# Kernel optimization log

Hardware: AMD Instinct MI355X
Metric: run time of the kernel (lower is better)

Reference implementation:

```python
import jax, jax.numpy as jnp
import numpy as np

B, T, D, H, E, K = 8, 4096, 768, 3072, 4, 2


def setup_inputs() -> dict:
    key = jax.random.key(0)
    ks = jax.random.split(key, 7)
    s = 0.02
    return {
        "x": jax.random.normal(ks[0], (B, T, D), dtype=jnp.float32),
        "router_w": jax.random.normal(ks[1], (D, E), dtype=jnp.float32) * s,
        "router_b": jnp.zeros((E,), dtype=jnp.float32),
        "W1": jax.random.normal(ks[2], (E, D, H), dtype=jnp.float32) * s,
        "b1": jnp.zeros((E, H), dtype=jnp.float32),
        "W2": jax.random.normal(ks[3], (E, H, D), dtype=jnp.float32) * s,
        "b2": jnp.zeros((E, D), dtype=jnp.float32),
    }


def reference(x, router_w, router_b, W1, b1, W2, b2):
    # Router: softmax over experts, then top-k selection.
    logits = jnp.einsum('btd,de->bte', x, router_w) + router_b        # [B,T,E]
    probs = jax.nn.softmax(logits, axis=-1)                           # [B,T,E]
    topk_probs, topk_idx = jax.lax.top_k(probs, K)                    # [B,T,K]

    # Per-expert combine weight: sum of top-k probs assigned to expert e.
    onehot = jax.nn.one_hot(topk_idx, E, dtype=x.dtype)               # [B,T,K,E]
    w = jnp.einsum('btk,btke->bte', topk_probs, onehot)               # [B,T,E]

    # Expert FFNs (exact-erf GELU matches torch F.gelu default).
    out = jnp.zeros_like(x)
    for e in range(E):
        h = jax.nn.gelu(jnp.einsum('btd,dh->bth', x, W1[e]) + b1[e], approximate=False)
        y = jnp.einsum('bth,hd->btd', h, W2[e]) + b2[e]
        out = out + w[..., e:e + 1] * y

    # Load-balance loss: expert assignment counts (non-differentiable, from int idx).
    counts = onehot.sum(axis=(0, 1, 2))                               # [E]
    token_fraction = counts / counts.sum()
    router_prob_mean = probs.mean(axis=(0, 1))                        # [E]
    load_balance_loss = E * jnp.sum(router_prob_mean * token_fraction)
    return out, load_balance_loss
```

## Files before the change

### kernel.cpp

```cpp
#include <hip/hip_runtime.h>
#include <hip/hip_bf16.h>
#include <hip/hip_fp16.h>

#define N_TOK 32768
#define D_DIM 768
#define H_DIM 3072
#define E_NUM 4
#define MT_PAD (N_TOK + 512)

#define TILE_E 4096

typedef _Float16 f16_t;
typedef _Float16 f16x8 __attribute__((ext_vector_type(8)));
typedef float f32x4 __attribute__((ext_vector_type(4)));

__device__ __forceinline__ f16_t f2h(float f) { return (f16_t)f; }

__device__ __forceinline__ void gload16(const void* g, void* l) {
  __builtin_amdgcn_global_load_lds(
      (const __attribute__((address_space(1))) void*)g,
      (__attribute__((address_space(3))) void*)l,
      16, 0, 0);
}

__device__ __forceinline__ void pipe_barrier() {
  asm volatile("" ::: "memory");
  __builtin_amdgcn_sched_barrier(0);
  __builtin_amdgcn_s_barrier();
  __builtin_amdgcn_sched_barrier(0);
  asm volatile("" ::: "memory");
}

__device__ __forceinline__ int xcd_swizzle(int f, int nwg) {
  const int q = nwg >> 3, r = nwg & 7;
  const int xcd = f & 7, pos = f >> 3;
  return (xcd < r ? xcd * (q + 1) : r * (q + 1) + (xcd - r) * q) + pos;
}


__global__ __launch_bounds__(256) void fill_kernel(unsigned* __restrict__ idx0,
                                                   unsigned* __restrict__ idx1) {
  const int t = blockIdx.x * 256 + threadIdx.x;
  for (int i = t; i < MT_PAD; i += gridDim.x * 256) {
    idx0[i] = 0xFFFFFFFFu;
    idx1[i] = 0xFFFFFFFFu;
  }
}

__global__ __launch_bounds__(256) void transform_kernel(
    const float* __restrict__ in, f16_t* __restrict__ outT,
    int R, int C, int NT, int KT) {
  __shared__ float tile[32][33];
  const int ez = blockIdx.z;
  in += (size_t)ez * R * C;
  const int c0 = blockIdx.x * 32, r0 = blockIdx.y * 32;
  const int tc = threadIdx.x & 31, tr = threadIdx.x >> 5;
#pragma unroll
  for (int i = 0; i < 32; i += 8)
    tile[tr + i][tc] = in[(size_t)(r0 + tr + i) * C + c0 + tc];
  __syncthreads();
  const int kt = r0 >> 5, g = tc >> 3, kk = tc & 7;
#pragma unroll
  for (int i = 0; i < 32; i += 8) {
    const int n = c0 + tr + i;
    const int nt = n >> 7, rl = n & 127;
    outT[(((size_t)(ez * NT + nt)) * KT + kt) * TILE_E + g * 1024 + rl * 8 + kk]
        = f2h(tile[tc][tr + i]);
  }
}

__global__ __launch_bounds__(256) void router_kernel(
    const float* __restrict__ x, const float* __restrict__ rw, const float* __restrict__ rb,
    float* __restrict__ wcomb, int* __restrict__ pairinfo,
    float* __restrict__ psum_part, int* __restrict__ cnt_part,
    int* __restrict__ cnt0_part, int* __restrict__ cnt1_part) {
  __shared__ float rwT[E_NUM][D_DIM];
  __shared__ float prW[4][E_NUM];
  __shared__ int   cnW[4][E_NUM];
  __shared__ int   cn0W[4][E_NUM];
  __shared__ int   cn1W[4][E_NUM];
  const int tid = threadIdx.x;
  for (int i = tid; i < D_DIM * E_NUM; i += 256) {
    int k = i >> 2, e = i & 3;
    rwT[e][k] = rw[i];
  }
  __syncthreads();
  const int lane = tid & 63, wv_ = tid >> 6;
  float pacc[E_NUM] = {0.f, 0.f, 0.f, 0.f};
  int   cacc[E_NUM] = {0, 0, 0, 0};
  int   c0acc[E_NUM] = {0, 0, 0, 0};
  int   c1acc[E_NUM] = {0, 0, 0, 0};
  const int tok0 = blockIdx.x * 32 + wv_ * 8;
  for (int t = 0; t < 8; ++t) {
    const int m = tok0 + t;
    const float* xr = x + (size_t)m * D_DIM;
    float s0 = 0.f, s1 = 0.f, s2 = 0.f, s3 = 0.f;
#pragma unroll
    for (int i = 0; i < D_DIM / 64; ++i) {
      int k = lane + i * 64;
      float xv = xr[k];
      s0 += xv * rwT[0][k]; s1 += xv * rwT[1][k];
      s2 += xv * rwT[2][k]; s3 += xv * rwT[3][k];
    }
#pragma unroll
    for (int off = 32; off >= 1; off >>= 1) {
      s0 += __shfl_xor(s0, off); s1 += __shfl_xor(s1, off);
      s2 += __shfl_xor(s2, off); s3 += __shfl_xor(s3, off);
    }
    if (lane == 0) {
      float lg[4] = {s0 + rb[0], s1 + rb[1], s2 + rb[2], s3 + rb[3]};
      float mx = fmaxf(fmaxf(lg[0], lg[1]), fmaxf(lg[2], lg[3]));
      float p[4]; float den = 0.f;
#pragma unroll
      for (int e = 0; e < 4; ++e) { p[e] = expf(lg[e] - mx); den += p[e]; }
      float inv = 1.f / den;
#pragma unroll
      for (int e = 0; e < 4; ++e) p[e] *= inv;
      int i1 = 0;
#pragma unroll
      for (int e = 1; e < 4; ++e) if (p[e] > p[i1]) i1 = e;
      int i2 = (i1 == 0) ? 1 : 0;
#pragma unroll
      for (int e = 0; e < 4; ++e) if (e != i1 && p[e] > p[i2]) i2 = e;
      float4 wvout;
      wvout.x = (0 == i1 || 0 == i2) ? p[0] : 0.f;
      wvout.y = (1 == i1 || 1 == i2) ? p[1] : 0.f;
      wvout.z = (2 == i1 || 2 == i2) ? p[2] : 0.f;
      wvout.w = (3 == i1 || 3 == i2) ? p[3] : 0.f;
      ((float4*)wcomb)[m] = wvout;
      const int emin = (i1 < i2) ? i1 : i2;
      const int emax = (i1 < i2) ? i2 : i1;
      pairinfo[m] = emin | (emax << 4);
      c0acc[emin]++; c1acc[emax]++;
#pragma unroll
      for (int e = 0; e < 4; ++e) pacc[e] += p[e];
      cacc[i1]++; cacc[i2]++;
    }
  }
  if (lane == 0) {
#pragma unroll
    for (int e = 0; e < 4; ++e) {
      prW[wv_][e] = pacc[e]; cnW[wv_][e] = cacc[e];
      cn0W[wv_][e] = c0acc[e]; cn1W[wv_][e] = c1acc[e];
    }
  }
  __syncthreads();
  if (tid < 4) {
    float ps = prW[0][tid] + prW[1][tid] + prW[2][tid] + prW[3][tid];
    int   cs = cnW[0][tid] + cnW[1][tid] + cnW[2][tid] + cnW[3][tid];
    psum_part[blockIdx.x * 4 + tid] = ps;
    cnt_part[blockIdx.x * 4 + tid]  = cs;
    cnt0_part[blockIdx.x * 4 + tid] = cn0W[0][tid] + cn0W[1][tid] + cn0W[2][tid] + cn0W[3][tid];
    cnt1_part[blockIdx.x * 4 + tid] = cn1W[0][tid] + cn1W[1][tid] + cn1W[2][tid] + cn1W[3][tid];
  }
}

__global__ void loss_kernel(const float* __restrict__ psum_part,
                            const int* __restrict__ cnt_part,
                            float* __restrict__ loss_out, int nblk) {
  const int lane = threadIdx.x;
  float ps[4] = {0.f, 0.f, 0.f, 0.f};
  int   cs[4] = {0, 0, 0, 0};
  for (int r = lane; r < nblk; r += 64) {
#pragma unroll
    for (int e = 0; e < 4; ++e) { ps[e] += psum_part[r * 4 + e]; cs[e] += cnt_part[r * 4 + e]; }
  }
#pragma unroll
  for (int off = 32; off >= 1; off >>= 1) {
#pragma unroll
    for (int e = 0; e < 4; ++e) {
      ps[e] += __shfl_xor(ps[e], off);
      cs[e] += __shfl_xor(cs[e], off);
    }
  }
  if (lane == 0) {
    float loss = 0.f;
#pragma unroll
    for (int e = 0; e < 4; ++e) {
      float mean = ps[e] / (float)N_TOK;
      float frac = (float)cs[e] / (float)(N_TOK * 2);
      loss += mean * frac;
    }
    loss_out[0] = 4.f * loss;
  }
}

__global__ __launch_bounds__(256) void setup_kernel(const int* __restrict__ cnt0_part,
                                                    const int* __restrict__ cnt1_part,
                                                    int* __restrict__ meta, int nblk) {
  __shared__ int sh[8][32];
  const int ch = threadIdx.x >> 5, ln = threadIdx.x & 31;
  const int* src = (ch < 4) ? cnt0_part : cnt1_part;
  const int e = ch & 3;
  int s = 0;
  for (int b = ln; b < nblk; b += 32) s += src[b * 4 + e];
  sh[ch][ln] = s;
  __syncthreads();
  if (threadIdx.x == 0) {
    int c[8];
    for (int c2 = 0; c2 < 8; ++c2) {
      int t = 0;
      for (int l = 0; l < 32; ++l) t += sh[c2][l];
      c[c2] = t;
    }
    int pb = 0; meta[8] = 0;
    for (int e2 = 0; e2 < 4; ++e2) { pb += (c[e2] + 127) & ~127; meta[9 + e2] = pb; }
    pb = 0; meta[13] = 0;
    for (int e2 = 0; e2 < 4; ++e2) { pb += (c[4 + e2] + 127) & ~127; meta[14 + e2] = pb; }
    for (int e2 = 0; e2 < 4; ++e2) { meta[18 + e2] = meta[8 + e2]; meta[22 + e2] = meta[13 + e2]; }
  }
}

__global__ __launch_bounds__(256) void scatter_kernel(const int* __restrict__ pairinfo,
                                                      int* __restrict__ meta,
                                                      unsigned* __restrict__ idx0,
                                                      unsigned* __restrict__ idx1) {
  __shared__ int wcnt[2][4][4];
  __shared__ int blkbase[2][4];
  const int tid = threadIdx.x, lane = tid & 63, wv = tid >> 6;
  const int t = blockIdx.x * 256 + tid;
  const int info = pairinfo[t];
  const int esel0 = info & 15, esel1 = info >> 4;
  int rank0 = 0, rank1 = 0;
#pragma unroll
  for (int e = 0; e < 4; ++e) {
    unsigned long long m0 = __ballot(esel0 == e);
    if (esel0 == e) rank0 = __popcll(m0 & ((1ull << lane) - 1ull));
    unsigned long long m1 = __ballot(esel1 == e);
    if (esel1 == e) rank1 = __popcll(m1 & ((1ull << lane) - 1ull));
    if (lane == 0) { wcnt[0][wv][e] = __popcll(m0); wcnt[1][wv][e] = __popcll(m1); }
  }
  __syncthreads();
  int wbase0 = 0, wbase1 = 0;
  for (int w = 0; w < wv; ++w) { wbase0 += wcnt[0][w][esel0]; wbase1 += wcnt[1][w][esel1]; }
  if (tid < 8) {
    const int p = tid >> 2, e = tid & 3;
    const int tot = wcnt[p][0][e] + wcnt[p][1][e] + wcnt[p][2][e] + wcnt[p][3][e];
    blkbase[p][e] = atomicAdd(&meta[(p ? 22 : 18) + e], tot);
  }
  __syncthreads();
  idx0[blkbase[0][esel0] + wbase0 + rank0] = (unsigned)t;
  idx1[blkbase[1][esel1] + wbase1 + rank1] = (unsigned)t;
}

__global__ __launch_bounds__(256) void gather_kernel(
    const float* __restrict__ x, const unsigned* __restrict__ idx_p,
    f16_t* __restrict__ xg, int srow) {
  __shared__ unsigned idx_s[128];
  const int tid = threadIdx.x, mt = blockIdx.x;
  if (tid < 128) {
    const int gr = srow + mt * 128 + tid;
    idx_s[tid] = (gr < MT_PAD) ? idx_p[gr] : 0xFFFFFFFFu;
  }
  __syncthreads();
  f16_t* dst = xg + (size_t)mt * 24 * TILE_E;
  for (int i = tid; i < 128 * 96; i += 256) {
    const int r = i / 96, grp = i - r * 96;
    const unsigned v = idx_s[r];
    const float* src = x + (size_t)((v < N_TOK) ? v : 0u) * D_DIM + grp * 8;
    float4 f0 = ((const float4*)src)[0];
    float4 f1 = ((const float4*)src)[1];
    f16x8 h;
    h[0] = f2h(f0.x); h[1] = f2h(f0.y); h[2] = f2h(f0.z); h[3] = f2h(f0.w);
    h[4] = f2h(f1.x); h[5] = f2h(f1.y); h[6] = f2h(f1.z); h[7] = f2h(f1.w);
    const int kt = grp >> 2, g = grp & 3;
    *(f16x8*)&dst[(size_t)kt * TILE_E + g * 1024 + r * 8] = h;
  }
}

#define BM 128
#define BN 128
#define BK 32

__global__ __launch_bounds__(256, 4) void gemm1_kernel(
    const f16_t* __restrict__ xg, const f16_t* __restrict__ W1T,
    const float* __restrict__ b1, const int* __restrict__ pb_p,
    f16_t* __restrict__ HwP, int srow) {
  __shared__ __align__(16) f16_t As[2][TILE_E];
  __shared__ __align__(16) f16_t Bs[2][TILE_E];
  const int tid = threadIdx.x, lane = tid & 63, wid = tid >> 6;
  const int wg = xcd_swizzle(blockIdx.x, gridDim.x);
  const int ntile = wg % 24, mtile = wg / 24;
  const int m128 = srow + mtile * BM;
  if (m128 >= pb_p[4]) return;
  int e = 0;
  while (e < 3 && m128 >= pb_p[e + 1]) ++e;
  const int n0 = ntile * BN;

  const f16_t* abase = xg + (size_t)mtile * 24 * TILE_E + lane * 8;
  const f16_t* bbase = W1T + (size_t)(e * 24 + ntile) * 24 * TILE_E + lane * 8;

  auto stage = [&](int buf, int kt) {
    const f16_t* a = abase + (size_t)kt * TILE_E;
    const f16_t* b = bbase + (size_t)kt * TILE_E;
    gload16(a + wid * 512,        &As[buf][wid * 512]);
    gload16(a + 2048 + wid * 512, &As[buf][2048 + wid * 512]);
    gload16(b + wid * 512,        &Bs[buf][wid * 512]);
    gload16(b + 2048 + wid * 512, &Bs[buf][2048 + wid * 512]);
  };

  const int wr = wid >> 1, wc = wid & 1;
  f32x4 acc[4][4] = {};

  float b1v[4];
#pragma unroll
  for (int nf = 0; nf < 4; ++nf)
    b1v[nf] = b1[e * H_DIM + n0 + wc * 64 + nf * 16 + (lane & 15)];

  stage(0, 0);
  stage(1, 1);
  int cur = 0;
  const int NT = D_DIM / BK;
  for (int t = 0; t < NT; ++t) {
    if (t + 1 < NT) { asm volatile("s_waitcnt vmcnt(4)" ::: "memory"); }
    else            { asm volatile("s_waitcnt vmcnt(0)" ::: "memory"); }
    pipe_barrier();
    const f16x8* Av = (const f16x8*)As[cur];
    const f16x8* Bv = (const f16x8*)Bs[cur];
    const int gsel = (lane >> 4) * 128;
    f16x8 a[4], b[4];
#pragma unroll
    for (int mf = 0; mf < 4; ++mf) a[mf] = Av[gsel + wr * 64 + mf * 16 + (lane & 15)];
#pragma unroll
    for (int nf = 0; nf < 4; ++nf) b[nf] = Bv[gsel + wc * 64 + nf * 16 + (lane & 15)];
#pragma unroll
    for (int mf = 0; mf < 4; ++mf)
#pragma unroll
      for (int nf = 0; nf < 4; ++nf)
        acc[mf][nf] = __builtin_amdgcn_mfma_f32_16x16x32_f16(a[mf], b[nf], acc[mf][nf], 0, 0, 0);
    pipe_barrier();
    if (t + 2 < NT) stage(cur, t + 2);
    cur ^= 1;
  }

  const int colb = wc * 64 + (lane & 15);
#pragma unroll
  for (int mf = 0; mf < 4; ++mf) {
    const int rowb = wr * 64 + mf * 16 + ((lane >> 4) << 2);
#pragma unroll
    for (int nf = 0; nf < 4; ++nf) {
      const int col = n0 + colb + nf * 16;
      const int kt = col >> 5, g = (col >> 3) & 3, kk = col & 7;
#pragma unroll
      for (int j = 0; j < 4; ++j) {
        const int row = rowb + j;
        float v = acc[mf][nf][j] + b1v[nf];
        float gel = 0.5f * v * (1.0f + erff(v * 0.70710678118654752440f));
        HwP[((size_t)(mtile * 96 + kt)) * TILE_E + g * 1024 + row * 8 + kk] = f2h(gel);
      }
    }
  }
}

__global__ __launch_bounds__(256, 4) void gemm2_kernel(
    const f16_t* __restrict__ HwP, const f16_t* __restrict__ W2T,
    const float* __restrict__ b2, const float* __restrict__ wcomb,
    const unsigned* __restrict__ idx_p, const int* __restrict__ pb_p,
    float* __restrict__ out, int srow, int doAdd) {
  __shared__ __align__(16) f16_t As[2][TILE_E];
  __shared__ __align__(16) f16_t Bs[2][TILE_E];
  __shared__ unsigned idx_s[BM];
  __shared__ float w_s[BM];
  const int tid = threadIdx.x, lane = tid & 63, wid = tid >> 6;
  const int wg = xcd_swizzle(blockIdx.x, gridDim.x);
  const int ntile = wg % 6, mtile = wg / 6;
  const int m128 = srow + mtile * BM;
  if (m128 >= pb_p[4]) return;
  int e = 0;
  while (e < 3 && m128 >= pb_p[e + 1]) ++e;
  const int n0 = ntile * BN;

  if (tid < BM) idx_s[tid] = idx_p[m128 + tid];
  __syncthreads();
  if (tid < BM) {
    unsigned v = idx_s[tid];
    w_s[tid] = (v < N_TOK) ? wcomb[v * 4 + e] : 0.f;
  }

  const f16_t* abase = HwP + (size_t)mtile * 96 * TILE_E + lane * 8;
  const f16_t* bbase = W2T + (size_t)(e * 6 + ntile) * 96 * TILE_E + lane * 8;

  auto stage = [&](int buf, int kt) {
    const f16_t* a = abase + (size_t)kt * TILE_E;
    const f16_t* b = bbase + (size_t)kt * TILE_E;
    gload16(a + wid * 512,        &As[buf][wid * 512]);
    gload16(a + 2048 + wid * 512, &As[buf][2048 + wid * 512]);
    gload16(b + wid * 512,        &Bs[buf][wid * 512]);
    gload16(b + 2048 + wid * 512, &Bs[buf][2048 + wid * 512]);
  };

  const int wr = wid >> 1, wc = wid & 1;
  f32x4 acc[4][4] = {};

  float b2v[4];
#pragma unroll
  for (int nf = 0; nf < 4; ++nf)
    b2v[nf] = b2[e * D_DIM + n0 + wc * 64 + nf * 16 + (lane & 15)];

  stage(0, 0);
  stage(1, 1);
  int cur = 0;
  const int NT = H_DIM / BK;
  for (int t = 0; t < NT; ++t) {
    if (t + 1 < NT) { asm volatile("s_waitcnt vmcnt(4)" ::: "memory"); }
    else            { asm volatile("s_waitcnt vmcnt(0)" ::: "memory"); }
    pipe_barrier();
    const f16x8* Av = (const f16x8*)As[cur];
    const f16x8* Bv = (const f16x8*)Bs[cur];
    const int gsel = (lane >> 4) * 128;
    f16x8 a[4], b[4];
#pragma unroll
    for (int mf = 0; mf < 4; ++mf) a[mf] = Av[gsel + wr * 64 + mf * 16 + (lane & 15)];
#pragma unroll
    for (int nf = 0; nf < 4; ++nf) b[nf] = Bv[gsel + wc * 64 + nf * 16 + (lane & 15)];
#pragma unroll
    for (int mf = 0; mf < 4; ++mf)
#pragma unroll
      for (int nf = 0; nf < 4; ++nf)
        acc[mf][nf] = __builtin_amdgcn_mfma_f32_16x16x32_f16(a[mf], b[nf], acc[mf][nf], 0, 0, 0);
    pipe_barrier();
    if (t + 2 < NT) stage(cur, t + 2);
    cur ^= 1;
  }

  const int colb = wc * 64 + (lane & 15);
#pragma unroll
  for (int mf = 0; mf < 4; ++mf) {
    const int rowb = wr * 64 + mf * 16 + ((lane >> 4) << 2);
#pragma unroll
    for (int nf = 0; nf < 4; ++nf) {
      const int col = n0 + colb + nf * 16;
#pragma unroll
      for (int j = 0; j < 4; ++j) {
        const int row = rowb + j;
        const unsigned v = idx_s[row];
        if (v < N_TOK) {
          float contrib = w_s[row] * (acc[mf][nf][j] + b2v[nf]);
          float* po = out + (size_t)v * D_DIM + col;
          if (doAdd) *po += contrib; else *po = contrib;
        }
      }
    }
  }
}

extern "C" void kernel_launch(void* const* d_in, const int* in_sizes, int n_in,
                              void* d_out, int out_size, void* d_ws, size_t ws_size,
                              hipStream_t stream) {
  const float* x  = (const float*)d_in[0];
  const float* rw = (const float*)d_in[1];
  const float* rb = (const float*)d_in[2];
  const float* W1 = (const float*)d_in[3];
  const float* b1 = (const float*)d_in[4];
  const float* W2 = (const float*)d_in[5];
  const float* b2 = (const float*)d_in[6];
  float* out = (float*)d_out;

  char* ws = (char*)d_ws;
  size_t off = 0;
  auto alloc = [&](size_t bytes) -> void* {
    void* p = ws + off;
    off = (off + bytes + 255) & ~(size_t)255;
    return p;
  };
  f16_t* W1T = (f16_t*)alloc((size_t)E_NUM * D_DIM * H_DIM * sizeof(f16_t));
  f16_t* W2T = (f16_t*)alloc((size_t)E_NUM * D_DIM * H_DIM * sizeof(f16_t));
  float* wcomb = (float*)alloc((size_t)N_TOK * E_NUM * sizeof(float));
  float* psum_part = (float*)alloc((size_t)(N_TOK / 32) * 4 * sizeof(float));
  int*   cnt_part  = (int*)alloc((size_t)(N_TOK / 32) * 4 * sizeof(int));
  int*   cnt0_part = (int*)alloc((size_t)(N_TOK / 32) * 4 * sizeof(int));
  int*   cnt1_part = (int*)alloc((size_t)(N_TOK / 32) * 4 * sizeof(int));
  int*   pairinfo  = (int*)alloc((size_t)N_TOK * sizeof(int));
  int*   meta      = (int*)alloc(32 * sizeof(int));
  unsigned* idx0   = (unsigned*)alloc((size_t)MT_PAD * sizeof(unsigned));
  unsigned* idx1   = (unsigned*)alloc((size_t)MT_PAD * sizeof(unsigned));

  size_t avail = (ws_size > off) ? ws_size - off : 0;
  int hwrows = (int)(avail / 7680);
  if (hwrows > MT_PAD) hwrows = MT_PAD;
  hwrows &= ~127;
  if (hwrows < 128) hwrows = 128;
  const int chunks = (MT_PAD + hwrows - 1) / hwrows;
  f16_t* xg  = (f16_t*)(ws + off);
  f16_t* HwP = (f16_t*)(ws + off + (size_t)hwrows * D_DIM * sizeof(f16_t));

  const int nblk = N_TOK / 32;

  fill_kernel<<<128, 256, 0, stream>>>(idx0, idx1);
  transform_kernel<<<dim3(H_DIM / 32, D_DIM / 32, E_NUM), 256, 0, stream>>>(W1, W1T, D_DIM, H_DIM, 24, 24);
  transform_kernel<<<dim3(D_DIM / 32, H_DIM / 32, E_NUM), 256, 0, stream>>>(W2, W2T, H_DIM, D_DIM, 6, 96);
  router_kernel<<<nblk, 256, 0, stream>>>(x, rw, rb, wcomb, pairinfo,
                                          psum_part, cnt_part, cnt0_part, cnt1_part);
  loss_kernel<<<1, 64, 0, stream>>>(psum_part, cnt_part, out + (size_t)N_TOK * D_DIM, nblk);
  setup_kernel<<<1, 256, 0, stream>>>(cnt0_part, cnt1_part, meta, nblk);
  scatter_kernel<<<N_TOK / 256, 256, 0, stream>>>(pairinfo, meta, idx0, idx1);

  for (int pass = 0; pass < 2; ++pass) {
    const unsigned* ip = pass ? idx1 : idx0;
    const int* pbp = meta + (pass ? 13 : 8);
    for (int c = 0; c < chunks; ++c) {
      const int srow = c * hwrows;
      gather_kernel<<<hwrows / BM, 256, 0, stream>>>(x, ip, xg, srow);
      gemm1_kernel<<<(hwrows / BM) * 24, 256, 0, stream>>>(xg, W1T, b1, pbp, HwP, srow);
      gemm2_kernel<<<(hwrows / BM) * 6, 256, 0, stream>>>(HwP, W2T, b2, wcomb, ip, pbp, out, srow, pass);
    }
  }
}
```

Measured before the change: 1.094 ms.

## Use 256-row M tiles for second-pass down-projection GEMM with 512-thread blocks

Adds a gemm2b kernel used on the second routing pass. It processes 256 token rows per block with 8 waves, so each staged W2 tile is reused across twice as many rows. Expert segment padding and chunk sizes are raised to multiples of 256 so no tile straddles two experts. The extra padding adds some wasted rows, and the larger blocks use more LDS, which may lower occupancy.

```diff
diff --git a/kernel.cpp b/kernel.cpp
--- a/kernel.cpp
+++ b/kernel.cpp
@@ -6,7 +6,7 @@
 #define D_DIM 768
 #define H_DIM 3072
 #define E_NUM 4
-#define MT_PAD (N_TOK + 512)
+#define MT_PAD (N_TOK + 1024)
 
 #define TILE_E 4096
 
@@ -204,9 +204,9 @@
       c[c2] = t;
     }
     int pb = 0; meta[8] = 0;
-    for (int e2 = 0; e2 < 4; ++e2) { pb += (c[e2] + 127) & ~127; meta[9 + e2] = pb; }
+    for (int e2 = 0; e2 < 4; ++e2) { pb += (c[e2] + 255) & ~255; meta[9 + e2] = pb; }
     pb = 0; meta[13] = 0;
-    for (int e2 = 0; e2 < 4; ++e2) { pb += (c[4 + e2] + 127) & ~127; meta[14 + e2] = pb; }
+    for (int e2 = 0; e2 < 4; ++e2) { pb += (c[4 + e2] + 255) & ~255; meta[14 + e2] = pb; }
     for (int e2 = 0; e2 < 4; ++e2) { meta[18 + e2] = meta[8 + e2]; meta[22 + e2] = meta[13 + e2]; }
   }
 }
@@ -438,6 +438,98 @@
           float contrib = w_s[row] * (acc[mf][nf][j] + b2v[nf]);
           float* po = out + (size_t)v * D_DIM + col;
           if (doAdd) *po += contrib; else *po = contrib;
+        }
+      }
+    }
+  }
+}
+
+__global__ __launch_bounds__(512, 4) void gemm2b_kernel(
+    const f16_t* __restrict__ HwP, const f16_t* __restrict__ W2T,
+    const float* __restrict__ b2, const float* __restrict__ wcomb,
+    const unsigned* __restrict__ idx_p, const int* __restrict__ pb_p,
+    float* __restrict__ out, int srow) {
+  __shared__ __align__(16) f16_t As[2][2 * TILE_E];
+  __shared__ __align__(16) f16_t Bs[2][TILE_E];
+  __shared__ unsigned idx_s[256];
+  __shared__ float w_s[256];
+  const int tid = threadIdx.x, lane = tid & 63, wid = tid >> 6;
+  const int wg = xcd_swizzle(blockIdx.x, gridDim.x);
+  const int ntile = wg % 6, mtile = wg / 6;
+  const int m256 = srow + mtile * 256;
+  if (m256 >= pb_p[4]) return;
+  int e = 0;
+  while (e < 3 && m256 >= pb_p[e + 1]) ++e;
+  const int n0 = ntile * BN;
+
+  if (tid < 256) idx_s[tid] = idx_p[m256 + tid];
+  __syncthreads();
+  if (tid < 256) {
+    unsigned v = idx_s[tid];
+    w_s[tid] = (v < N_TOK) ? wcomb[v * 4 + e] : 0.f;
+  }
+
+  const f16_t* apan = HwP + ((size_t)(2 * mtile) + (wid >> 2)) * 96 * TILE_E + lane * 8;
+  const int aoff = (wid & 3) * 1024;
+  const f16_t* bbase = W2T + (size_t)(e * 6 + ntile) * 96 * TILE_E + lane * 8;
+
+  auto stage = [&](int buf, int kt) {
+    const f16_t* a = apan + (size_t)kt * TILE_E + aoff;
+    gload16(a,       &As[buf][(wid >> 2) * TILE_E + aoff]);
+    gload16(a + 512, &As[buf][(wid >> 2) * TILE_E + aoff + 512]);
+    const f16_t* b = bbase + (size_t)kt * TILE_E + wid * 512;
+    gload16(b, &Bs[buf][wid * 512]);
+  };
+
+  const int wr = wid >> 1, wc = wid & 1;
+  f32x4 acc[4][4] = {};
+
+  float b2v[4];
+#pragma unroll
+  for (int nf = 0; nf < 4; ++nf)
+    b2v[nf] = b2[e * D_DIM + n0 + wc * 64 + nf * 16 + (lane & 15)];
+
+  stage(0, 0);
+  stage(1, 1);
+  int cur = 0;
+  const int NT = H_DIM / BK;
+  for (int t = 0; t < NT; ++t) {
+    if (t + 1 < NT) { asm volatile("s_waitcnt vmcnt(3)" ::: "memory"); }
+    else            { asm volatile("s_waitcnt vmcnt(0)" ::: "memory"); }
+    pipe_barrier();
+    const f16x8* Av = (const f16x8*)&As[cur][(wr >> 1) * TILE_E];
+    const f16x8* Bv = (const f16x8*)Bs[cur];
+    const int wrl = wr & 1;
+    const int gsel = (lane >> 4) * 128;
+    f16x8 a[4], b[4];
+#pragma unroll
+    for (int mf = 0; mf < 4; ++mf) a[mf] = Av[gsel + wrl * 64 + mf * 16 + (lane & 15)];
+#pragma unroll
+    for (int nf = 0; nf < 4; ++nf) b[nf] = Bv[gsel + wc * 64 + nf * 16 + (lane & 15)];
+#pragma unroll
+    for (int mf = 0; mf < 4; ++mf)
+#pragma unroll
+      for (int nf = 0; nf < 4; ++nf)
+        acc[mf][nf] = __builtin_amdgcn_mfma_f32_16x16x32_f16(a[mf], b[nf], acc[mf][nf], 0, 0, 0);
+    pipe_barrier();
+    if (t + 2 < NT) stage(cur, t + 2);
+    cur ^= 1;
+  }
+
+  const int colb = wc * 64 + (lane & 15);
+#pragma unroll
+  for (int mf = 0; mf < 4; ++mf) {
+    const int rowb = wr * 64 + mf * 16 + ((lane >> 4) << 2);
+#pragma unroll
+    for (int nf = 0; nf < 4; ++nf) {
+      const int col = n0 + colb + nf * 16;
+#pragma unroll
+      for (int j = 0; j < 4; ++j) {
+        const int row = rowb + j;
+        const unsigned v = idx_s[row];
+        if (v < N_TOK) {
+          float contrib = w_s[row] * (acc[mf][nf][j] + b2v[nf]);
+          out[(size_t)v * D_DIM + col] += contrib;
         }
       }
     }
@@ -478,8 +570,8 @@
   size_t avail = (ws_size > off) ? ws_size - off : 0;
   int hwrows = (int)(avail / 7680);
   if (hwrows > MT_PAD) hwrows = MT_PAD;
-  hwrows &= ~127;
-  if (hwrows < 128) hwrows = 128;
+  hwrows &= ~255;
+  if (hwrows < 256) hwrows = 256;
   const int chunks = (MT_PAD + hwrows - 1) / hwrows;
   f16_t* xg  = (f16_t*)(ws + off);
   f16_t* HwP = (f16_t*)(ws + off + (size_t)hwrows * D_DIM * sizeof(f16_t));
@@ -500,9 +592,13 @@
     const int* pbp = meta + (pass ? 13 : 8);
     for (int c = 0; c < chunks; ++c) {
       const int srow = c * hwrows;
-      gather_kernel<<<hwrows / BM, 256, 0, stream>>>(x, ip, xg, srow);
-      gemm1_kernel<<<(hwrows / BM) * 24, 256, 0, stream>>>(xg, W1T, b1, pbp, HwP, srow);
-      gemm2_kernel<<<(hwrows / BM) * 6, 256, 0, stream>>>(HwP, W2T, b2, wcomb, ip, pbp, out, srow, pass);
-    }
-  }
-}
+      gather_kernel<<<hwrows / 128, 256, 0, stream>>>(x, ip, xg, srow);
+      gemm1_kernel<<<(hwrows / 128) * 24, 256, 0, stream>>>(xg, W1T, b1, pbp, HwP, srow);
+      if (pass == 0) {
+        gemm2_kernel<<<(hwrows / 128) * 6, 256, 0, stream>>>(HwP, W2T, b2, wcomb, ip, pbp, out, srow, 0);
+      } else {
+        gemm2b_kernel<<<(hwrows / 256) * 6, 512, 0, stream>>>(HwP, W2T, b2, wcomb, ip, pbp, out, srow);
+      }
+    }
+  }
+}
```

After: 1.108 ms. No clear change (+1.2%).
